# Performance work log

Hardware: AMD Instinct MI355X
Metric: run time of the kernel (lower is better)

The kernel has to match this reference:

```python
import jax, jax.numpy as jnp
import numpy as np

NUM_HEADS = 12

def setup_inputs() -> dict:
    key = jax.random.key(0)
    ks = jax.random.split(key, 6)
    B_, N, C = 4096, 49, 384
    return {
        'x': jax.random.normal(ks[0], (B_, N, C), dtype=jnp.float32),
        'mask': jax.random.normal(ks[1], (B_, N, N), dtype=jnp.float32),
        'qkv_w': jax.random.normal(ks[2], (3 * C, C), dtype=jnp.float32) * 0.02,
        'qkv_b': jax.random.normal(ks[3], (3 * C,), dtype=jnp.float32) * 0.02,
        'proj_w': jax.random.normal(ks[4], (C, C), dtype=jnp.float32) * 0.02,
        'proj_b': jax.random.normal(ks[5], (C,), dtype=jnp.float32) * 0.02,
    }

def reference(x, mask, qkv_w, qkv_b, proj_w, proj_b):
    B_, N, C = x.shape
    H = NUM_HEADS
    D = C // H
    scale = 1.0 / (D ** 0.5)
    # fused QKV projection: [B_, N, 3, H, D] -> [3, B_, H, N, D]
    qkv = (x @ qkv_w.T + qkv_b).reshape(B_, N, 3, H, D)
    qkv = jnp.transpose(qkv, (2, 0, 3, 1, 4))
    q, k, v = qkv[0], qkv[1], qkv[2]
    attn = jnp.einsum('bhnd,bhmd->bhnm', q, k) * scale
    attn = attn + mask[:, None, :, :]  # broadcast over heads
    attn = jax.nn.softmax(attn, axis=-1)
    out = jnp.einsum('bhnm,bhmd->bhnd', attn, v)
    out = jnp.transpose(out, (0, 2, 1, 3)).reshape(B_, N, C)
    return out @ proj_w.T + proj_b
```

## Files before the change

kernel.cpp:

```cpp
#include <hip/hip_runtime.h>
#include <hip/hip_bf16.h>
#include <cstdint>
#include <cstddef>


typedef __bf16 bf16_t;
typedef __bf16 bf16x8 __attribute__((ext_vector_type(8)));
typedef __bf16 bf16x4 __attribute__((ext_vector_type(4)));
typedef float  floatx4 __attribute__((ext_vector_type(4)));

#define MFMA16(a, b, c) __builtin_amdgcn_mfma_f32_16x16x32_bf16((a), (b), (c), 0, 0, 0)

static const int CH   = 384;
static const int MTOT = 200704;

__global__ void cvt_kernel(const float* __restrict__ src, bf16_t* __restrict__ dst) {
    int i = (blockIdx.x * 256 + threadIdx.x) * 4;
    float4 v = *(const float4*)(src + i);
    bf16x4 o;
    o[0] = (bf16_t)v.x; o[1] = (bf16_t)v.y; o[2] = (bf16_t)v.z; o[3] = (bf16_t)v.w;
    *(bf16x4*)(dst + i) = o;
}

__global__ __launch_bounds__(256) void qkv_kernel(
    const bf16_t* __restrict__ xb, const bf16_t* __restrict__ wb,
    const float* __restrict__ bias,
    bf16_t* __restrict__ qb, bf16_t* __restrict__ kb, bf16_t* __restrict__ vb)
{
    __shared__ __align__(16) bf16_t As[128][40];
    __shared__ __align__(16) bf16_t Bs[128][40];
    const int tid  = threadIdx.x;
    const int lane = tid & 63, wave = tid >> 6;
    const int quad = lane >> 4, l15 = lane & 15;
    const int m0 = blockIdx.x * 128, j0 = blockIdx.y * 128;
    const int wrow = (wave & 1) * 64, wcol = (wave >> 1) * 64;
    const int srow = tid >> 2, sc = (tid & 3) * 8;

    floatx4 acc[4][4];
#pragma unroll
    for (int a = 0; a < 4; ++a)
#pragma unroll
        for (int b2 = 0; b2 < 4; ++b2)
#pragma unroll
            for (int r = 0; r < 4; ++r) acc[a][b2][r] = 0.f;

    for (int kt = 0; kt < 12; ++kt) {
        const int k0 = kt * 32;
        *(bf16x8*)&As[srow][sc]      = *(const bf16x8*)&xb[(size_t)(m0 + srow) * CH + k0 + sc];
        *(bf16x8*)&As[srow + 64][sc] = *(const bf16x8*)&xb[(size_t)(m0 + srow + 64) * CH + k0 + sc];
        *(bf16x8*)&Bs[srow][sc]      = *(const bf16x8*)&wb[(size_t)(j0 + srow) * CH + k0 + sc];
        *(bf16x8*)&Bs[srow + 64][sc] = *(const bf16x8*)&wb[(size_t)(j0 + srow + 64) * CH + k0 + sc];
        __syncthreads();
        bf16x8 af[4], bfr[4];
#pragma unroll
        for (int mt = 0; mt < 4; ++mt) af[mt]  = *(const bf16x8*)&As[wrow + mt * 16 + l15][quad * 8];
#pragma unroll
        for (int nt = 0; nt < 4; ++nt) bfr[nt] = *(const bf16x8*)&Bs[wcol + nt * 16 + l15][quad * 8];
#pragma unroll
        for (int mt = 0; mt < 4; ++mt)
#pragma unroll
            for (int nt = 0; nt < 4; ++nt)
                acc[mt][nt] = MFMA16(af[mt], bfr[nt], acc[mt][nt]);
        __syncthreads();
    }

    const int t = j0 / CH;
#pragma unroll
    for (int mt = 0; mt < 4; ++mt)
#pragma unroll
        for (int nt = 0; nt < 4; ++nt)
#pragma unroll
            for (int r = 0; r < 4; ++r) {
                unsigned m = (unsigned)(m0 + wrow + mt * 16 + quad * 4 + r);
                unsigned j = (unsigned)(j0 + wcol + nt * 16 + l15);
                float val = acc[mt][nt][r] + bias[j];
                unsigned b = m / 49u, n = m % 49u;
                unsigned jr = j - (unsigned)(t * CH);
                unsigned h = jr >> 5, d = jr & 31u;
                size_t bh = (size_t)b * 12u + h;
                if (t == 0)      qb[(bh * 49u + n) * 32u + d] = (bf16_t)(val * 0.17677669529663687f);
                else if (t == 1) kb[(bh * 49u + n) * 32u + d] = (bf16_t)val;
                else             vb[(bh * 32u + d) * 64u + n] = (bf16_t)val;
            }
}

__global__ __launch_bounds__(256) void attn_kernel(
    const bf16_t* __restrict__ qb, const bf16_t* __restrict__ kb,
    const bf16_t* __restrict__ vb, const float* __restrict__ mask,
    bf16_t* __restrict__ ao)
{
    __shared__ __align__(16) bf16_t S[4][64][72];
    __shared__ float rsum[4][64];
    const int tid  = threadIdx.x;
    const int w = tid >> 6, lane = tid & 63;
    const int quad = lane >> 4, l15 = lane & 15;
    const unsigned gw = blockIdx.x * 4u + (unsigned)w;
    const unsigned b = gw / 12u, h = gw % 12u;
    const bf16_t* qh = qb + (size_t)gw * 1568u;
    const bf16_t* kh = kb + (size_t)gw * 1568u;
    const bf16_t* vh = vb + (size_t)gw * 2048u;

    bf16x8 qf[4], kf[4];
#pragma unroll
    for (int mt = 0; mt < 4; ++mt) qf[mt] = *(const bf16x8*)&qh[(mt * 16 + l15) * 32 + quad * 8];
#pragma unroll
    for (int nt = 0; nt < 4; ++nt) kf[nt] = *(const bf16x8*)&kh[(nt * 16 + l15) * 32 + quad * 8];
    floatx4 sacc[4][4];
#pragma unroll
    for (int a = 0; a < 4; ++a)
#pragma unroll
        for (int c = 0; c < 4; ++c)
#pragma unroll
            for (int r = 0; r < 4; ++r) sacc[a][c][r] = 0.f;
#pragma unroll
    for (int mt = 0; mt < 4; ++mt)
#pragma unroll
        for (int nt = 0; nt < 4; ++nt)
            sacc[mt][nt] = MFMA16(qf[mt], kf[nt], sacc[mt][nt]);

#pragma unroll
    for (int mt = 0; mt < 4; ++mt)
#pragma unroll
        for (int nt = 0; nt < 4; ++nt)
#pragma unroll
            for (int r = 0; r < 4; ++r)
                S[w][mt * 16 + quad * 4 + r][nt * 16 + l15] = (bf16_t)sacc[mt][nt][r];
    __syncthreads();

    const int r = lane;
    if (r < 49) {
        const float* mrow = mask + ((size_t)b * 49u + (unsigned)r) * 49u;
        float mx = -1e30f;
#pragma unroll
        for (int ch = 0; ch < 7; ++ch) {
            bf16x8 v = *(const bf16x8*)&S[w][r][ch * 8];
#pragma unroll
            for (int jj = 0; jj < 8; ++jj) {
                int c = ch * 8 + jj;
                if (c < 49) mx = fmaxf(mx, (float)v[jj] + mrow[c]);
            }
        }
        float sum = 0.f;
#pragma unroll
        for (int ch = 0; ch < 7; ++ch) {
            bf16x8 v = *(const bf16x8*)&S[w][r][ch * 8];
            bf16x8 pv;
#pragma unroll
            for (int jj = 0; jj < 8; ++jj) {
                int c = ch * 8 + jj;
                float p = 0.f;
                if (c < 49) { p = __expf((float)v[jj] + mrow[c] - mx); sum += p; }
                pv[jj] = (bf16_t)p;
            }
            *(bf16x8*)&S[w][r][ch * 8] = pv;
        }
        bf16x8 z;
#pragma unroll
        for (int jj = 0; jj < 8; ++jj) z[jj] = (bf16_t)0.f;
        *(bf16x8*)&S[w][r][56] = z;
        rsum[w][r] = 1.f / sum;
    }
    __syncthreads();

    floatx4 oacc[4][2];
#pragma unroll
    for (int a = 0; a < 4; ++a)
#pragma unroll
        for (int c = 0; c < 2; ++c)
#pragma unroll
            for (int rr = 0; rr < 4; ++rr) oacc[a][c][rr] = 0.f;
#pragma unroll
    for (int kt = 0; kt < 2; ++kt) {
        bf16x8 pf[4], vf[2];
#pragma unroll
        for (int mt = 0; mt < 4; ++mt) pf[mt] = *(const bf16x8*)&S[w][mt * 16 + l15][kt * 32 + quad * 8];
#pragma unroll
        for (int nt = 0; nt < 2; ++nt) vf[nt] = *(const bf16x8*)&vh[(nt * 16 + l15) * 64 + kt * 32 + quad * 8];
#pragma unroll
        for (int mt = 0; mt < 4; ++mt)
#pragma unroll
            for (int nt = 0; nt < 2; ++nt)
                oacc[mt][nt] = MFMA16(pf[mt], vf[nt], oacc[mt][nt]);
    }
#pragma unroll
    for (int mt = 0; mt < 4; ++mt)
#pragma unroll
        for (int nt = 0; nt < 2; ++nt)
#pragma unroll
            for (int rr = 0; rr < 4; ++rr) {
                int row = mt * 16 + quad * 4 + rr;
                if (row < 49) {
                    float val = oacc[mt][nt][rr] * rsum[w][row];
                    ao[((size_t)b * 49u + (unsigned)row) * 384u + h * 32u + (unsigned)(nt * 16 + l15)] = (bf16_t)val;
                }
            }
}

__global__ __launch_bounds__(256) void proj_kernel(
    const bf16_t* __restrict__ ab, const bf16_t* __restrict__ wb,
    const float* __restrict__ bias, float* __restrict__ out)
{
    __shared__ __align__(16) bf16_t As[128][40];
    __shared__ __align__(16) bf16_t Bs[128][40];
    const int tid  = threadIdx.x;
    const int lane = tid & 63, wave = tid >> 6;
    const int quad = lane >> 4, l15 = lane & 15;
    const int m0 = blockIdx.x * 128, j0 = blockIdx.y * 128;
    const int wrow = (wave & 1) * 64, wcol = (wave >> 1) * 64;
    const int srow = tid >> 2, sc = (tid & 3) * 8;

    floatx4 acc[4][4];
#pragma unroll
    for (int a = 0; a < 4; ++a)
#pragma unroll
        for (int b2 = 0; b2 < 4; ++b2)
#pragma unroll
            for (int r = 0; r < 4; ++r) acc[a][b2][r] = 0.f;

    for (int kt = 0; kt < 12; ++kt) {
        const int k0 = kt * 32;
        *(bf16x8*)&As[srow][sc]      = *(const bf16x8*)&ab[(size_t)(m0 + srow) * CH + k0 + sc];
        *(bf16x8*)&As[srow + 64][sc] = *(const bf16x8*)&ab[(size_t)(m0 + srow + 64) * CH + k0 + sc];
        *(bf16x8*)&Bs[srow][sc]      = *(const bf16x8*)&wb[(size_t)(j0 + srow) * CH + k0 + sc];
        *(bf16x8*)&Bs[srow + 64][sc] = *(const bf16x8*)&wb[(size_t)(j0 + srow + 64) * CH + k0 + sc];
        __syncthreads();
        bf16x8 af[4], bfr[4];
#pragma unroll
        for (int mt = 0; mt < 4; ++mt) af[mt]  = *(const bf16x8*)&As[wrow + mt * 16 + l15][quad * 8];
#pragma unroll
        for (int nt = 0; nt < 4; ++nt) bfr[nt] = *(const bf16x8*)&Bs[wcol + nt * 16 + l15][quad * 8];
#pragma unroll
        for (int mt = 0; mt < 4; ++mt)
#pragma unroll
            for (int nt = 0; nt < 4; ++nt)
                acc[mt][nt] = MFMA16(af[mt], bfr[nt], acc[mt][nt]);
        __syncthreads();
    }

#pragma unroll
    for (int mt = 0; mt < 4; ++mt)
#pragma unroll
        for (int nt = 0; nt < 4; ++nt)
#pragma unroll
            for (int r = 0; r < 4; ++r) {
                int m = m0 + wrow + mt * 16 + quad * 4 + r;
                int j = j0 + wcol + nt * 16 + l15;
                out[(size_t)m * CH + j] = acc[mt][nt][r] + bias[j];
            }
}

extern "C" void kernel_launch(void* const* d_in, const int* in_sizes, int n_in,
                              void* d_out, int out_size, void* d_ws, size_t ws_size,
                              hipStream_t stream) {
    const float* x      = (const float*)d_in[0];
    const float* mask   = (const float*)d_in[1];
    const float* qkv_w  = (const float*)d_in[2];
    const float* qkv_b  = (const float*)d_in[3];
    const float* proj_w = (const float*)d_in[4];
    const float* proj_b = (const float*)d_in[5];
    float* out = (float*)d_out;

    const size_t XB_B    = (size_t)77070336 * 2;
    const size_t QB_B    = (size_t)77070336 * 2;
    const size_t KB_B    = (size_t)77070336 * 2;
    const size_t VB_B    = (size_t)100663296 * 2;
    const size_t WQKV_B  = (size_t)442368 * 2;
    const size_t WPROJ_B = (size_t)147456 * 2;
    const size_t NEED = XB_B + QB_B + KB_B + VB_B + WQKV_B + WPROJ_B + 4096;
    if (ws_size < NEED) return;

    char* p = (char*)d_ws;
    bf16_t* xb     = (bf16_t*)p; p += XB_B;
    bf16_t* qb     = (bf16_t*)p; p += QB_B;
    bf16_t* kb     = (bf16_t*)p; p += KB_B;
    bf16_t* vb     = (bf16_t*)p; p += VB_B;
    bf16_t* wqkvb  = (bf16_t*)p; p += WQKV_B;
    bf16_t* wprojb = (bf16_t*)p;

    cvt_kernel<<<75264, 256, 0, stream>>>(x, xb);
    cvt_kernel<<<432, 256, 0, stream>>>(qkv_w, wqkvb);
    cvt_kernel<<<144, 256, 0, stream>>>(proj_w, wprojb);
    qkv_kernel<<<dim3(1568, 9), 256, 0, stream>>>(xb, wqkvb, qkv_b, qb, kb, vb);
    attn_kernel<<<12288, 256, 0, stream>>>(qb, kb, vb, mask, xb );
    proj_kernel<<<dim3(1568, 3), 256, 0, stream>>>(xb, wprojb, proj_b, out);
}
```

Baseline: 1.441 ms.

## Double-buffer GEMM tiles via direct global-to-LDS loads, fold mask into score accumulator

The QKV and projection GEMMs now load tiles straight into LDS with global_load_lds into two buffers, using an XOR swizzle in place of padding, so the next k-tile is fetched while MFMAs run on the current one. Explicit waitcnt and barriers replace __syncthreads. The attention kernel seeds the QK^T accumulator with mask values and groups each block's heads under one batch, which removes the mask reads from the softmax loop. The hand-placed vmcnt counts and barriers are fragile, and the attention epilogue now does more scattered loads.

```diff
diff --git a/kernel.cpp b/kernel.cpp
--- a/kernel.cpp
+++ b/kernel.cpp
@@ -13,6 +13,13 @@
 
 static const int CH   = 384;
 static const int MTOT = 200704;
+
+__device__ __forceinline__ void gload16(const bf16_t* g, bf16_t* l) {
+    __builtin_amdgcn_global_load_lds(
+        (const __attribute__((address_space(1))) unsigned int*)g,
+        (__attribute__((address_space(3))) unsigned int*)l,
+        16, 0, 0);
+}
 
 __global__ void cvt_kernel(const float* __restrict__ src, bf16_t* __restrict__ dst) {
     int i = (blockIdx.x * 256 + threadIdx.x) * 4;
@@ -27,14 +34,13 @@
     const float* __restrict__ bias,
     bf16_t* __restrict__ qb, bf16_t* __restrict__ kb, bf16_t* __restrict__ vb)
 {
-    __shared__ __align__(16) bf16_t As[128][40];
-    __shared__ __align__(16) bf16_t Bs[128][40];
+    __shared__ __align__(16) bf16_t As[2][128 * 32];
+    __shared__ __align__(16) bf16_t Bs[2][128 * 32];
     const int tid  = threadIdx.x;
     const int lane = tid & 63, wave = tid >> 6;
     const int quad = lane >> 4, l15 = lane & 15;
     const int m0 = blockIdx.x * 128, j0 = blockIdx.y * 128;
     const int wrow = (wave & 1) * 64, wcol = (wave >> 1) * 64;
-    const int srow = tid >> 2, sc = (tid & 3) * 8;
 
     floatx4 acc[4][4];
 #pragma unroll
@@ -44,37 +50,61 @@
 #pragma unroll
             for (int r = 0; r < 4; ++r) acc[a][b2][r] = 0.f;
 
+#define QKV_STAGE(KT, BI)                                                          \
+    do {                                                                           \
+        const int k0s = (KT) * 32;                                                 \
+        _Pragma("unroll")                                                          \
+        for (int rd = 0; rd < 2; ++rd) {                                           \
+            int c = rd * 256 + tid;                                                \
+            int row = c >> 2, p = c & 3;                                           \
+            int q = p ^ ((row >> 1) & 3);                                          \
+            gload16(xb + (size_t)(m0 + row) * CH + k0s + q * 8, &As[BI][c * 8]);   \
+            gload16(wb + (size_t)(j0 + row) * CH + k0s + q * 8, &Bs[BI][c * 8]);   \
+        }                                                                          \
+    } while (0)
+
+    QKV_STAGE(0, 0);
+#pragma unroll
     for (int kt = 0; kt < 12; ++kt) {
-        const int k0 = kt * 32;
-        *(bf16x8*)&As[srow][sc]      = *(const bf16x8*)&xb[(size_t)(m0 + srow) * CH + k0 + sc];
-        *(bf16x8*)&As[srow + 64][sc] = *(const bf16x8*)&xb[(size_t)(m0 + srow + 64) * CH + k0 + sc];
-        *(bf16x8*)&Bs[srow][sc]      = *(const bf16x8*)&wb[(size_t)(j0 + srow) * CH + k0 + sc];
-        *(bf16x8*)&Bs[srow + 64][sc] = *(const bf16x8*)&wb[(size_t)(j0 + srow + 64) * CH + k0 + sc];
-        __syncthreads();
+        const int cur = kt & 1;
+        if (kt < 11) {
+            QKV_STAGE(kt + 1, cur ^ 1);
+            asm volatile("s_waitcnt vmcnt(4)" ::: "memory");
+        } else {
+            asm volatile("s_waitcnt vmcnt(0)" ::: "memory");
+        }
+        __builtin_amdgcn_sched_barrier(0);
+        __builtin_amdgcn_s_barrier();
         bf16x8 af[4], bfr[4];
 #pragma unroll
-        for (int mt = 0; mt < 4; ++mt) af[mt]  = *(const bf16x8*)&As[wrow + mt * 16 + l15][quad * 8];
-#pragma unroll
-        for (int nt = 0; nt < 4; ++nt) bfr[nt] = *(const bf16x8*)&Bs[wcol + nt * 16 + l15][quad * 8];
+        for (int mt = 0; mt < 4; ++mt) {
+            int rA = wrow + mt * 16 + l15;
+            af[mt]  = *(const bf16x8*)&As[cur][rA * 32 + (quad ^ ((rA >> 1) & 3)) * 8];
+            int rB = wcol + mt * 16 + l15;
+            bfr[mt] = *(const bf16x8*)&Bs[cur][rB * 32 + (quad ^ ((rB >> 1) & 3)) * 8];
+        }
 #pragma unroll
         for (int mt = 0; mt < 4; ++mt)
 #pragma unroll
             for (int nt = 0; nt < 4; ++nt)
                 acc[mt][nt] = MFMA16(af[mt], bfr[nt], acc[mt][nt]);
-        __syncthreads();
+        asm volatile("s_waitcnt lgkmcnt(0)" ::: "memory");
+        __builtin_amdgcn_sched_barrier(0);
+        __builtin_amdgcn_s_barrier();
     }
+#undef QKV_STAGE
 
     const int t = j0 / CH;
 #pragma unroll
     for (int mt = 0; mt < 4; ++mt)
 #pragma unroll
-        for (int nt = 0; nt < 4; ++nt)
-#pragma unroll
-            for (int r = 0; r < 4; ++r) {
-                unsigned m = (unsigned)(m0 + wrow + mt * 16 + quad * 4 + r);
+        for (int r = 0; r < 4; ++r) {
+            unsigned m = (unsigned)(m0 + wrow + mt * 16 + quad * 4 + r);
+            unsigned b = m / 49u, n = m % 49u;
+#pragma unroll
+            for (int nt = 0; nt < 4; ++nt) {
                 unsigned j = (unsigned)(j0 + wcol + nt * 16 + l15);
                 float val = acc[mt][nt][r] + bias[j];
-                unsigned b = m / 49u, n = m % 49u;
                 unsigned jr = j - (unsigned)(t * CH);
                 unsigned h = jr >> 5, d = jr & 31u;
                 size_t bh = (size_t)b * 12u + h;
@@ -82,6 +112,7 @@
                 else if (t == 1) kb[(bh * 49u + n) * 32u + d] = (bf16_t)val;
                 else             vb[(bh * 32u + d) * 64u + n] = (bf16_t)val;
             }
+        }
 }
 
 __global__ __launch_bounds__(256) void attn_kernel(
@@ -94,11 +125,13 @@
     const int tid  = threadIdx.x;
     const int w = tid >> 6, lane = tid & 63;
     const int quad = lane >> 4, l15 = lane & 15;
-    const unsigned gw = blockIdx.x * 4u + (unsigned)w;
-    const unsigned b = gw / 12u, h = gw % 12u;
+    const unsigned b = blockIdx.x / 3u;
+    const unsigned h = (blockIdx.x % 3u) * 4u + (unsigned)w;
+    const unsigned gw = b * 12u + h;
     const bf16_t* qh = qb + (size_t)gw * 1568u;
     const bf16_t* kh = kb + (size_t)gw * 1568u;
     const bf16_t* vh = vb + (size_t)gw * 2048u;
+    const float*  mb = mask + (size_t)b * 2401u;
 
     bf16x8 qf[4], kf[4];
 #pragma unroll
@@ -107,11 +140,19 @@
     for (int nt = 0; nt < 4; ++nt) kf[nt] = *(const bf16x8*)&kh[(nt * 16 + l15) * 32 + quad * 8];
     floatx4 sacc[4][4];
 #pragma unroll
-    for (int a = 0; a < 4; ++a)
-#pragma unroll
-        for (int c = 0; c < 4; ++c)
-#pragma unroll
-            for (int r = 0; r < 4; ++r) sacc[a][c][r] = 0.f;
+    for (int mt = 0; mt < 4; ++mt)
+#pragma unroll
+        for (int r = 0; r < 4; ++r) {
+            int rr = mt * 16 + quad * 4 + r;
+            const float* mrow = mb + rr * 49;
+#pragma unroll
+            for (int nt = 0; nt < 4; ++nt) {
+                int col = nt * 16 + l15;
+                float mval = 0.f;
+                if (rr < 49) mval = mrow[col < 49 ? col : 48];
+                sacc[mt][nt][r] = mval;
+            }
+        }
 #pragma unroll
     for (int mt = 0; mt < 4; ++mt)
 #pragma unroll
@@ -129,7 +170,6 @@
 
     const int r = lane;
     if (r < 49) {
-        const float* mrow = mask + ((size_t)b * 49u + (unsigned)r) * 49u;
         float mx = -1e30f;
 #pragma unroll
         for (int ch = 0; ch < 7; ++ch) {
@@ -137,7 +177,7 @@
 #pragma unroll
             for (int jj = 0; jj < 8; ++jj) {
                 int c = ch * 8 + jj;
-                if (c < 49) mx = fmaxf(mx, (float)v[jj] + mrow[c]);
+                if (c < 49) mx = fmaxf(mx, (float)v[jj]);
             }
         }
         float sum = 0.f;
@@ -149,7 +189,7 @@
             for (int jj = 0; jj < 8; ++jj) {
                 int c = ch * 8 + jj;
                 float p = 0.f;
-                if (c < 49) { p = __expf((float)v[jj] + mrow[c] - mx); sum += p; }
+                if (c < 49) { p = __expf((float)v[jj] - mx); sum += p; }
                 pv[jj] = (bf16_t)p;
             }
             *(bf16x8*)&S[w][r][ch * 8] = pv;
@@ -200,14 +240,13 @@
     const bf16_t* __restrict__ ab, const bf16_t* __restrict__ wb,
     const float* __restrict__ bias, float* __restrict__ out)
 {
-    __shared__ __align__(16) bf16_t As[128][40];
-    __shared__ __align__(16) bf16_t Bs[128][40];
+    __shared__ __align__(16) bf16_t As[2][128 * 32];
+    __shared__ __align__(16) bf16_t Bs[2][128 * 32];
     const int tid  = threadIdx.x;
     const int lane = tid & 63, wave = tid >> 6;
     const int quad = lane >> 4, l15 = lane & 15;
     const int m0 = blockIdx.x * 128, j0 = blockIdx.y * 128;
     const int wrow = (wave & 1) * 64, wcol = (wave >> 1) * 64;
-    const int srow = tid >> 2, sc = (tid & 3) * 8;
 
     floatx4 acc[4][4];
 #pragma unroll
@@ -217,25 +256,49 @@
 #pragma unroll
             for (int r = 0; r < 4; ++r) acc[a][b2][r] = 0.f;
 
+#define PROJ_STAGE(KT, BI)                                                         \
+    do {                                                                           \
+        const int k0s = (KT) * 32;                                                 \
+        _Pragma("unroll")                                                          \
+        for (int rd = 0; rd < 2; ++rd) {                                           \
+            int c = rd * 256 + tid;                                                \
+            int row = c >> 2, p = c & 3;                                           \
+            int q = p ^ ((row >> 1) & 3);                                          \
+            gload16(ab + (size_t)(m0 + row) * CH + k0s + q * 8, &As[BI][c * 8]);   \
+            gload16(wb + (size_t)(j0 + row) * CH + k0s + q * 8, &Bs[BI][c * 8]);   \
+        }                                                                          \
+    } while (0)
+
+    PROJ_STAGE(0, 0);
+#pragma unroll
     for (int kt = 0; kt < 12; ++kt) {
-        const int k0 = kt * 32;
-        *(bf16x8*)&As[srow][sc]      = *(const bf16x8*)&ab[(size_t)(m0 + srow) * CH + k0 + sc];
-        *(bf16x8*)&As[srow + 64][sc] = *(const bf16x8*)&ab[(size_t)(m0 + srow + 64) * CH + k0 + sc];
-        *(bf16x8*)&Bs[srow][sc]      = *(const bf16x8*)&wb[(size_t)(j0 + srow) * CH + k0 + sc];
-        *(bf16x8*)&Bs[srow + 64][sc] = *(const bf16x8*)&wb[(size_t)(j0 + srow + 64) * CH + k0 + sc];
-        __syncthreads();
+        const int cur = kt & 1;
+        if (kt < 11) {
+            PROJ_STAGE(kt + 1, cur ^ 1);
+            asm volatile("s_waitcnt vmcnt(4)" ::: "memory");
+        } else {
+            asm volatile("s_waitcnt vmcnt(0)" ::: "memory");
+        }
+        __builtin_amdgcn_sched_barrier(0);
+        __builtin_amdgcn_s_barrier();
         bf16x8 af[4], bfr[4];
 #pragma unroll
-        for (int mt = 0; mt < 4; ++mt) af[mt]  = *(const bf16x8*)&As[wrow + mt * 16 + l15][quad * 8];
-#pragma unroll
-        for (int nt = 0; nt < 4; ++nt) bfr[nt] = *(const bf16x8*)&Bs[wcol + nt * 16 + l15][quad * 8];
+        for (int mt = 0; mt < 4; ++mt) {
+            int rA = wrow + mt * 16 + l15;
+            af[mt]  = *(const bf16x8*)&As[cur][rA * 32 + (quad ^ ((rA >> 1) & 3)) * 8];
+            int rB = wcol + mt * 16 + l15;
+            bfr[mt] = *(const bf16x8*)&Bs[cur][rB * 32 + (quad ^ ((rB >> 1) & 3)) * 8];
+        }
 #pragma unroll
         for (int mt = 0; mt < 4; ++mt)
 #pragma unroll
             for (int nt = 0; nt < 4; ++nt)
                 acc[mt][nt] = MFMA16(af[mt], bfr[nt], acc[mt][nt]);
-        __syncthreads();
+        asm volatile("s_waitcnt lgkmcnt(0)" ::: "memory");
+        __builtin_amdgcn_sched_barrier(0);
+        __builtin_amdgcn_s_barrier();
     }
+#undef PROJ_STAGE
 
 #pragma unroll
     for (int mt = 0; mt < 4; ++mt)
```

New measurement: 1.267 ms. 1.14x faster.
